# Performance work log

Hardware: AMD Instinct MI355X
Metric: run time of the kernel (lower is better)

The kernel has to match this reference:

```python
import jax, jax.numpy as jnp
import numpy as np

EPS = 1e-8

def setup_inputs() -> dict:
    key = jax.random.key(0)
    ks = jax.random.split(key, 10)
    N, IN, Z, C, H = 8192, 512, 128, 64, 50
    x = jax.random.normal(ks[0], (N, IN), dtype=jnp.float32)
    c = jax.random.randint(ks[1], (N, 1), 0, C, dtype=jnp.int64)
    z = jax.random.normal(ks[2], (N, Z), dtype=jnp.float32)
    # f_x MLP params (Linear(IN,50) -> ReLU -> Linear(50,Z))
    W1 = jax.random.normal(ks[3], (IN, H), dtype=jnp.float32) / np.sqrt(IN)
    b1 = jax.random.normal(ks[4], (H,), dtype=jnp.float32) * 0.01
    W2 = jax.random.normal(ks[5], (H, Z), dtype=jnp.float32) / np.sqrt(H)
    b2 = jax.random.normal(ks[6], (Z,), dtype=jnp.float32) * 0.01
    # f_z Linear(Z,Z)
    Wz = jax.random.normal(ks[7], (Z, Z), dtype=jnp.float32) / np.sqrt(Z)
    bz = jax.random.normal(ks[8], (Z,), dtype=jnp.float32) * 0.01
    # per-category bilinear weights w_s [C,Z,Z] (torch.randn init)
    Ws = jax.random.normal(ks[9], (C, Z, Z), dtype=jnp.float32)
    return {"x": x, "c": c, "z": z, "W1": W1, "b1": b1, "W2": W2, "b2": b2, "Wz": Wz, "bz": bz, "Ws": Ws}

def reference(x, c, z, W1, b1, W2, b2, Wz, bz, Ws):
    cf = c.reshape(-1)                                    # [N]
    fx = jax.nn.relu(x @ W1 + b1) @ W2 + b2               # [N,Z]
    fz = z @ Wz + bz                                      # [N,Z]
    # per-sample bilinear: u[n] = fx[n] @ Ws[c[n]]
    u = jnp.einsum('nd,nde->ne', fx, Ws[cf])              # [N,Z]
    T = jax.nn.softplus(jnp.einsum('ne,ne->n', u, fz))    # [N]
    # neg_T[i] = mean over j with c[j]==c[i] of softplus(fx[i] @ Ws[c[i]] @ fz[j])
    S = jax.nn.softplus(u @ fz.T)                         # [N,N]
    mask = (cf[:, None] == cf[None, :]).astype(S.dtype)   # [N,N]
    neg_T = (S * mask).sum(axis=1) / mask.sum(axis=1)     # [N]
    return jnp.log(T + EPS) - jnp.log(neg_T + EPS)
```

## Files before the change

### kernel.cpp

```cpp
#include <hip/hip_runtime.h>
#include <math.h>

#define N_   8192
#define IN_  512
#define ZD   128
#define CC   64
#define HD   50
#define EPSF 1e-8f

typedef float vf4 __attribute__((ext_vector_type(4)));
typedef __attribute__((ext_vector_type(8))) short bfrag;

#define MFMA16(a, b, c) __builtin_amdgcn_mfma_f32_16x16x32_bf16((a), (b), (c), 0, 0, 0)

__device__ __forceinline__ float softplus_hot(float t) {
    return fmaxf(t, 0.f) + __logf(1.f + __expf(-fabsf(t)));
}
__device__ __forceinline__ float softplus_acc(float t) {
    return fmaxf(t, 0.f) + log1pf(expf(-fabsf(t)));
}
__device__ __forceinline__ unsigned short bf16_rn(float x) {
    unsigned int u = __float_as_uint(x);
    return (unsigned short)((u + 0x7fff + ((u >> 16) & 1)) >> 16);
}
__device__ __forceinline__ float bf16_f(unsigned short h) {
    return __uint_as_float(((unsigned int)h) << 16);
}
__device__ __forceinline__ void split8(const float* v, bfrag& hi, bfrag& lo) {
    #pragma unroll
    for (int e = 0; e < 8; ++e) {
        unsigned short h = bf16_rn(v[e]);
        ((short*)&hi)[e] = (short)h;
        ((short*)&lo)[e] = (short)bf16_rn(v[e] - bf16_f(h));
    }
}

__global__ __launch_bounds__(256) void k_pre(const int* __restrict__ c,
                                             const float* __restrict__ W1,
                                             const float* __restrict__ z,
                                             const float* __restrict__ Wz,
                                             const float* __restrict__ bz,
                                             const float* __restrict__ W2,
                                             const float* __restrict__ Ws,
                                             uint4* __restrict__ W1p,
                                             uint4* __restrict__ W2p,
                                             float* __restrict__ fz,
                                             unsigned short* __restrict__ fz_hi,
                                             unsigned short* __restrict__ Wst_hi,
                                             unsigned short* __restrict__ Wst_lo,
                                             int* __restrict__ counts,
                                             int* __restrict__ offsets,
                                             int* __restrict__ grouped) {
    __shared__ float smem[64 * 129];
    int tid = threadIdx.x;
    int b   = blockIdx.x;
    if (b < CC) {
        __shared__ int hist[CC];
        __shared__ int cursor;
        __shared__ int off_s;
        if (tid < CC) hist[tid] = 0;
        if (tid == 0) cursor = 0;
        __syncthreads();
        for (int i = tid; i < N_; i += 256) atomicAdd(&hist[c[i]], 1);
        __syncthreads();
        if (tid == 0) {
            int off = 0;
            for (int q = 0; q < b; ++q) off += hist[q];
            off_s = off;
            counts[b]  = hist[b];
            offsets[b] = off;
        }
        __syncthreads();
        int off = off_s;
        for (int i = tid; i < N_; i += 256) {
            if (c[i] == b) {
                int p = atomicAdd(&cursor, 1);
                grouped[off + p] = i;
            }
        }
    } else if (b < 80) {
        int unit = (b - 64) * 256 + tid;
        int lane = unit & 63, f = (unit >> 6) & 15, kc = unit >> 10;
        int nt = f >> 2, ks = f & 3;
        int n = nt * 16 + (lane & 15);
        int kbase = kc * 128 + ks * 32 + (lane >> 4) * 8;
        unsigned short hi8[8], lo8[8];
        #pragma unroll
        for (int j = 0; j < 8; ++j) {
            int k = kbase + j;
            float v = (n < HD) ? W1[k * HD + n] : 0.f;
            unsigned short h = bf16_rn(v);
            hi8[j] = h;
            lo8[j] = bf16_rn(v - bf16_f(h));
        }
        W1p[kc * 2048 + f * 64 + lane]        = *(uint4*)hi8;
        W1p[kc * 2048 + 1024 + f * 64 + lane] = *(uint4*)lo8;
    } else if (b < 84) {
        int unit = (b - 80) * 256 + tid;
        int lane = unit & 63, f = unit >> 6;
        int nt = f >> 1, ks = f & 1;
        int n = nt * 16 + (lane & 15);
        int kbase = ks * 32 + (lane >> 4) * 8;
        unsigned short hi8[8], lo8[8];
        #pragma unroll
        for (int j = 0; j < 8; ++j) {
            int k = kbase + j;
            float v = (k < HD) ? W2[k * ZD + n] : 0.f;
            unsigned short h = bf16_rn(v);
            hi8[j] = h;
            lo8[j] = bf16_rn(v - bf16_f(h));
        }
        W2p[f * 64 + lane]        = *(uint4*)hi8;
        W2p[1024 + f * 64 + lane] = *(uint4*)lo8;
    } else if (b < 212) {
        float* sz = smem;
        int row0 = (b - 84) * 64;
        vf4* s4 = (vf4*)sz;
        const vf4* z4 = (const vf4*)(z + (size_t)row0 * ZD);
        #pragma unroll
        for (int f = 0; f < 8; ++f) s4[tid + f * 256] = z4[tid + f * 256];
        __syncthreads();
        int cp = tid & 31, rgp = tid >> 5;
        const vf4* Wz4 = (const vf4*)Wz;
        vf4 bb = ((const vf4*)bz)[cp];
        vf4 acc[8];
        #pragma unroll
        for (int r = 0; r < 8; ++r) acc[r] = bb;
        #pragma unroll 1
        for (int d4 = 0; d4 < 32; ++d4) {
            vf4 w0 = Wz4[(4 * d4 + 0) * 32 + cp];
            vf4 w1 = Wz4[(4 * d4 + 1) * 32 + cp];
            vf4 w2 = Wz4[(4 * d4 + 2) * 32 + cp];
            vf4 w3 = Wz4[(4 * d4 + 3) * 32 + cp];
            #pragma unroll
            for (int r = 0; r < 8; ++r) {
                vf4 a = s4[(rgp * 8 + r) * 32 + d4];
                acc[r] += a[0] * w0;
                acc[r] += a[1] * w1;
                acc[r] += a[2] * w2;
                acc[r] += a[3] * w3;
            }
        }
        vf4* fz4 = (vf4*)fz;
        #pragma unroll
        for (int r = 0; r < 8; ++r) {
            int n = row0 + rgp * 8 + r;
            fz4[(size_t)n * 32 + cp] = acc[r];
            ushort4 h;
            h.x = bf16_rn(acc[r][0]); h.y = bf16_rn(acc[r][1]);
            h.z = bf16_rn(acc[r][2]); h.w = bf16_rn(acc[r][3]);
            *(ushort4*)(fz_hi + (size_t)n * ZD + cp * 4) = h;
        }
    } else {
        #pragma unroll 1
        for (int ci = 0; ci < 2; ++ci) {
            int cat = (b - 212) * 2 + ci;
            const float* Wc = Ws + (size_t)cat * ZD * ZD;
            unsigned short* Whi = Wst_hi + (size_t)cat * ZD * ZD;
            unsigned short* Wlo = Wst_lo + (size_t)cat * ZD * ZD;
            #pragma unroll 1
            for (int half = 0; half < 2; ++half) {
                __syncthreads();
                const vf4* src = (const vf4*)(Wc + (size_t)half * 64 * ZD);
                #pragma unroll
                for (int f = 0; f < 8; ++f) {
                    int idx = tid + f * 256;
                    int row = idx >> 5, q = idx & 31;
                    vf4 v = src[idx];
                    #pragma unroll
                    for (int e = 0; e < 4; ++e) smem[row * 129 + q * 4 + e] = v[e];
                }
                __syncthreads();
                #pragma unroll 1
                for (int f = 0; f < 32; ++f) {
                    int idx = tid + f * 256;
                    int e = idx >> 6, dd = idx & 63;
                    float v = smem[dd * 129 + e];
                    unsigned short h = bf16_rn(v);
                    Whi[(size_t)e * ZD + half * 64 + dd] = h;
                    Wlo[(size_t)e * ZD + half * 64 + dd] = bf16_rn(v - bf16_f(h));
                }
            }
        }
    }
}

#define TI 8
__global__ __launch_bounds__(512) void k_all(const float* __restrict__ x,
                                             const uint4* __restrict__ W1p,
                                             const uint4* __restrict__ W2p,
                                             const float* __restrict__ b1,
                                             const float* __restrict__ b2,
                                             const unsigned short* __restrict__ Wst_hi,
                                             const unsigned short* __restrict__ Wst_lo,
                                             const float* __restrict__ fz,
                                             const unsigned short* __restrict__ fz_hi,
                                             const int* __restrict__ grouped,
                                             const int* __restrict__ offsets,
                                             const int* __restrict__ counts,
                                             float* __restrict__ out) {
    __shared__ __align__(16) unsigned char SM[78848];
    uint4* A4    = (uint4*)(SM);
    uint4* B4    = (uint4*)(SM + 34816);
    float* shC   = (float*)(SM + 69632);
    float* sRedF = (float*)(SM + 78336);

    int tid = threadIdx.x;
    int cat = blockIdx.x >> 3;
    int t   = blockIdx.x & (TI - 1);
    int off = offsets[cat], cnt = counts[cat];
    int i0 = t * 32;
    if (i0 >= cnt) return;
    int mI = min(32, cnt - i0);

    int lane = tid & 63, wave = tid >> 6;
    int m = lane & 15, quad = lane >> 4;
    int rg = wave & 1, ch = wave >> 1;

    uint4* sW2 = A4;
    uint4* sW1 = B4;
    float* sh  = shC;

    #pragma unroll
    for (int f = 0; f < 4; ++f) sW2[tid + f * 512] = W2p[tid + f * 512];

    int irowA = rg * 16 + m;
    int n_gA = grouped[off + i0 + min(irowA, mI - 1)];
    const float4* xr = (const float4*)(x + (size_t)n_gA * IN_);

    vf4 accP = {0.f, 0.f, 0.f, 0.f};
    vf4 accQ = {0.f, 0.f, 0.f, 0.f};
    vf4 accR = {0.f, 0.f, 0.f, 0.f};

    #pragma unroll 1
    for (int kc = 0; kc < 4; ++kc) {
        __syncthreads();
        #pragma unroll
        for (int f = 0; f < 4; ++f)
            sW1[tid + f * 512] = W1p[kc * 2048 + tid + f * 512];
        __syncthreads();
        #pragma unroll 1
        for (int ks = 0; ks < 4; ++ks) {
            float4 xa = xr[kc * 32 + ks * 8 + quad * 2];
            float4 xb = xr[kc * 32 + ks * 8 + quad * 2 + 1];
            float xv[8] = {xa.x, xa.y, xa.z, xa.w, xb.x, xb.y, xb.z, xb.w};
            bfrag ah, al;
            split8(xv, ah, al);
            bfrag bh = *(const bfrag*)&sW1[(ch * 4 + ks) * 64 + lane];
            bfrag bl = *(const bfrag*)&sW1[1024 + (ch * 4 + ks) * 64 + lane];
            accP = MFMA16(ah, bh, accP);
            accQ = MFMA16(ah, bl, accQ);
            accR = MFMA16(al, bh, accR);
        }
    }
    {
        int col = ch * 16 + m;
        float bb = (col < HD) ? b1[col] : 0.f;
        vf4 acc = accP + accQ + accR;
        #pragma unroll
        for (int r = 0; r < 4; ++r)
            sh[(rg * 16 + quad * 4 + r) * 68 + col] = fmaxf(acc[r] + bb, 0.f);
    }
    __syncthreads();

    bfrag ah2[2], al2[2];
    #pragma unroll
    for (int ks = 0; ks < 2; ++ks) {
        const float4* shp = (const float4*)&sh[(rg * 16 + m) * 68 + ks * 32 + quad * 8];
        float4 ha = shp[0], hb = shp[1];
        float hv[8] = {ha.x, ha.y, ha.z, ha.w, hb.x, hb.y, hb.z, hb.w};
        split8(hv, ah2[ks], al2[ks]);
    }
    __syncthreads();

    unsigned short* fxhiT = (unsigned short*)shC;
    unsigned short* fxloT = (unsigned short*)B4;
    #pragma unroll
    for (int nt2 = 0; nt2 < 2; ++nt2) {
        int nt = ch * 2 + nt2;
        bfrag bh0 = *(const bfrag*)&sW2[(nt * 2 + 0) * 64 + lane];
        bfrag bl0 = *(const bfrag*)&sW2[1024 + (nt * 2 + 0) * 64 + lane];
        bfrag bh1 = *(const bfrag*)&sW2[(nt * 2 + 1) * 64 + lane];
        bfrag bl1 = *(const bfrag*)&sW2[1024 + (nt * 2 + 1) * 64 + lane];
        vf4 aA = {0.f, 0.f, 0.f, 0.f}, aB = {0.f, 0.f, 0.f, 0.f};
        aA = MFMA16(ah2[0], bh0, aA);
        aA = MFMA16(ah2[0], bl0, aA);
        aA = MFMA16(al2[0], bh0, aA);
        aB = MFMA16(ah2[1], bh1, aB);
        aB = MFMA16(ah2[1], bl1, aB);
        aB = MFMA16(al2[1], bh1, aB);
        vf4 a2 = aA + aB;
        int colB = nt * 16 + m;
        float bb2 = b2[colB];
        #pragma unroll
        for (int r = 0; r < 4; ++r) {
            int row = rg * 16 + quad * 4 + r;
            float v = a2[r] + bb2;
            unsigned short hh = bf16_rn(v);
            fxhiT[row * 136 + colB] = hh;
            fxloT[row * 136 + colB] = bf16_rn(v - bf16_f(hh));
        }
    }
    __syncthreads();

    int eh = ch;
    bfrag a_hi[4], a_lo[4];
    #pragma unroll
    for (int kb = 0; kb < 4; ++kb) {
        a_hi[kb] = *(const bfrag*)&fxhiT[(rg * 16 + m) * 136 + kb * 32 + quad * 8];
        a_lo[kb] = *(const bfrag*)&fxloT[(rg * 16 + m) * 136 + kb * 32 + quad * 8];
    }
    __syncthreads();

    uint4* sWhi = A4;
    uint4* sWlo = B4;
    const uint4* gh = (const uint4*)(Wst_hi + (size_t)cat * ZD * ZD);
    const uint4* gl = (const uint4*)(Wst_lo + (size_t)cat * ZD * ZD);
    #pragma unroll
    for (int f = 0; f < 4; ++f) {
        int idx = tid + f * 512;
        int e = idx >> 4, q = idx & 15;
        sWhi[e * 17 + q] = gh[idx];
        sWlo[e * 17 + q] = gl[idx];
    }
    __syncthreads();

    vf4 uacc[2];
    #pragma unroll 1
    for (int et2 = 0; et2 < 2; ++et2) {
        int et = eh * 2 + et2;
        vf4 aH = {0.f, 0.f, 0.f, 0.f};
        vf4 aM = {0.f, 0.f, 0.f, 0.f};
        vf4 aL = {0.f, 0.f, 0.f, 0.f};
        #pragma unroll
        for (int kb = 0; kb < 4; ++kb) {
            bfrag bh = *(const bfrag*)&sWhi[(et * 16 + m) * 17 + kb * 4 + quad];
            bfrag bl = *(const bfrag*)&sWlo[(et * 16 + m) * 17 + kb * 4 + quad];
            aH = MFMA16(a_hi[kb], bh, aH);
            aM = MFMA16(a_hi[kb], bl, aM);
            aL = MFMA16(a_lo[kb], bh, aL);
        }
        uacc[et2] = aH + aM + aL;
    }

    int nrow[4];
    #pragma unroll
    for (int r = 0; r < 4; ++r) {
        int ir = rg * 16 + quad * 4 + r;
        nrow[r] = (ir < mI) ? grouped[off + i0 + ir] : -1;
    }
    float fzv[2][4];
    #pragma unroll
    for (int et2 = 0; et2 < 2; ++et2) {
        #pragma unroll
        for (int r = 0; r < 4; ++r) {
            fzv[et2][r] = 0.f;
            if (nrow[r] >= 0)
                fzv[et2][r] = fz[(size_t)nrow[r] * ZD + (eh * 2 + et2) * 16 + m];
        }
    }
    float p[4] = {0.f, 0.f, 0.f, 0.f};
    #pragma unroll
    for (int et2 = 0; et2 < 2; ++et2) {
        #pragma unroll
        for (int r = 0; r < 4; ++r) p[r] += uacc[et2][r] * fzv[et2][r];
    }
    #pragma unroll
    for (int r = 0; r < 4; ++r) {
        float v = p[r];
        #pragma unroll
        for (int s = 8; s >= 1; s >>= 1) v += __shfl_xor(v, s, 64);
        p[r] = v;
    }
    if (m == 0) {
        #pragma unroll
        for (int r = 0; r < 4; ++r)
            sRedF[(rg * 4 + eh) * 16 + quad * 4 + r] = p[r];
    }
    __syncthreads();

    unsigned short* su = (unsigned short*)A4;
    #pragma unroll
    for (int et2 = 0; et2 < 2; ++et2) {
        int col = (eh * 2 + et2) * 16 + m;
        #pragma unroll
        for (int r = 0; r < 4; ++r)
            su[(rg * 16 + quad * 4 + r) * 136 + col] = bf16_rn(uacc[et2][r]);
    }
    float logT_r[4] = {0.f, 0.f, 0.f, 0.f};
    if (eh == 0) {
        #pragma unroll
        for (int r = 0; r < 4; ++r) {
            float pt = sRedF[(rg * 4 + 0) * 16 + quad * 4 + r]
                     + sRedF[(rg * 4 + 1) * 16 + quad * 4 + r]
                     + sRedF[(rg * 4 + 2) * 16 + quad * 4 + r]
                     + sRedF[(rg * 4 + 3) * 16 + quad * 4 + r];
            logT_r[r] = logf(softplus_acc(pt) + EPSF);
        }
    }
    __syncthreads();

    bfrag na[4];
    #pragma unroll
    for (int kb = 0; kb < 4; ++kb)
        na[kb] = *(const bfrag*)&su[(rg * 16 + m) * 136 + kb * 32 + quad * 8];

    uint4* sB = B4;
    float negsum[4] = {0.f, 0.f, 0.f, 0.f};

    #pragma unroll 1
    for (int jb = 0; jb < cnt; jb += 64) {
        int mJ = min(64, cnt - jb);
        __syncthreads();
        #pragma unroll
        for (int f = 0; f < 2; ++f) {
            int idx = tid + f * 512;
            int jr = idx >> 4, q = idx & 15;
            uint4 v = {0u, 0u, 0u, 0u};
            if (jr < mJ) {
                int j_g = grouped[off + jb + jr];
                v = *(const uint4*)(fz_hi + (size_t)j_g * ZD + q * 8);
            }
            sB[jr * 17 + q] = v;
        }
        __syncthreads();
        {
            int jt = eh;
            bfrag b0 = *(const bfrag*)&sB[(jt * 16 + m) * 17 + 0 + quad];
            bfrag b1 = *(const bfrag*)&sB[(jt * 16 + m) * 17 + 4 + quad];
            bfrag b2 = *(const bfrag*)&sB[(jt * 16 + m) * 17 + 8 + quad];
            bfrag b3 = *(const bfrag*)&sB[(jt * 16 + m) * 17 + 12 + quad];
            vf4 aA = {0.f, 0.f, 0.f, 0.f}, aB = {0.f, 0.f, 0.f, 0.f};
            aA = MFMA16(na[0], b0, aA);
            aA = MFMA16(na[1], b1, aA);
            aB = MFMA16(na[2], b2, aB);
            aB = MFMA16(na[3], b3, aB);
            vf4 acc = aA + aB;
            bool jok = (jt * 16 + m) < mJ;
            #pragma unroll
            for (int r = 0; r < 4; ++r)
                if (jok) negsum[r] += softplus_hot(acc[r]);
        }
    }

    #pragma unroll
    for (int r = 0; r < 4; ++r) {
        float v = negsum[r];
        #pragma unroll
        for (int s = 8; s >= 1; s >>= 1) v += __shfl_xor(v, s, 64);
        negsum[r] = v;
    }
    if (m == 0) {
        #pragma unroll
        for (int r = 0; r < 4; ++r)
            sRedF[(rg * 4 + eh) * 16 + quad * 4 + r] = negsum[r];
    }
    __syncthreads();
    if (eh == 0 && m == 0) {
        #pragma unroll
        for (int r = 0; r < 4; ++r) {
            if (nrow[r] >= 0) {
                float tot = sRedF[(rg * 4 + 0) * 16 + quad * 4 + r]
                          + sRedF[(rg * 4 + 1) * 16 + quad * 4 + r]
                          + sRedF[(rg * 4 + 2) * 16 + quad * 4 + r]
                          + sRedF[(rg * 4 + 3) * 16 + quad * 4 + r];
                out[nrow[r]] = logT_r[r] - logf(tot / (float)cnt + EPSF);
            }
        }
    }
}

extern "C" void kernel_launch(void* const* d_in, const int* in_sizes, int n_in,
                              void* d_out, int out_size, void* d_ws, size_t ws_size,
                              hipStream_t stream) {
    const float* x  = (const float*)d_in[0];
    const int*   c  = (const int*)  d_in[1];
    const float* z  = (const float*)d_in[2];
    const float* W1 = (const float*)d_in[3];
    const float* b1 = (const float*)d_in[4];
    const float* W2 = (const float*)d_in[5];
    const float* b2 = (const float*)d_in[6];
    const float* Wz = (const float*)d_in[7];
    const float* bz = (const float*)d_in[8];
    const float* Ws = (const float*)d_in[9];
    float* out = (float*)d_out;

    uint4* W1p = (uint4*)d_ws;
    uint4* W2p = W1p + 8192;
    float* fz  = (float*)(W2p + 2048);
    unsigned short* fz_hi  = (unsigned short*)(fz + (size_t)N_ * ZD);
    unsigned short* Wst_hi = fz_hi + (size_t)N_ * ZD;
    unsigned short* Wst_lo = Wst_hi + (size_t)CC * ZD * ZD;
    int* counts  = (int*)(Wst_lo + (size_t)CC * ZD * ZD);
    int* offsets = counts + CC;
    int* grouped = offsets + CC;

    k_pre <<<244, 256, 0, stream>>>(c, W1, z, Wz, bz, W2, Ws, W1p, W2p, fz,
                                    fz_hi, Wst_hi, Wst_lo, counts, offsets,
                                    grouped);
    k_all <<<CC * TI, 512, 0, stream>>>(x, W1p, W2p, b1, b2, Wst_hi, Wst_lo,
                                        fz, fz_hi, grouped, offsets, counts,
                                        out);
}
```

Before: 132.2 us.

## Prefetch fz tiles and W1 chunks into registers, split Ws conversion across more blocks

```diff
diff --git a/kernel.cpp b/kernel.cpp
--- a/kernel.cpp
+++ b/kernel.cpp
@@ -29,7 +29,8 @@
 __device__ __forceinline__ void split8(const float* v, bfrag& hi, bfrag& lo) {
     #pragma unroll
     for (int e = 0; e < 8; ++e) {
-        unsigned short h = bf16_rn(v[e]);
+        unsigned int u = __float_as_uint(v[e]);
+        unsigned short h = (unsigned short)(u >> 16);
         ((short*)&hi)[e] = (short)h;
         ((short*)&lo)[e] = (short)bf16_rn(v[e] - bf16_f(h));
     }
@@ -152,34 +153,31 @@
             *(ushort4*)(fz_hi + (size_t)n * ZD + cp * 4) = h;
         }
     } else {
+        int cat = b - 212;
+        const float* Wc = Ws + (size_t)cat * ZD * ZD;
+        unsigned short* Whi = Wst_hi + (size_t)cat * ZD * ZD;
+        unsigned short* Wlo = Wst_lo + (size_t)cat * ZD * ZD;
         #pragma unroll 1
-        for (int ci = 0; ci < 2; ++ci) {
-            int cat = (b - 212) * 2 + ci;
-            const float* Wc = Ws + (size_t)cat * ZD * ZD;
-            unsigned short* Whi = Wst_hi + (size_t)cat * ZD * ZD;
-            unsigned short* Wlo = Wst_lo + (size_t)cat * ZD * ZD;
+        for (int half = 0; half < 2; ++half) {
+            __syncthreads();
+            const vf4* src = (const vf4*)(Wc + (size_t)half * 64 * ZD);
+            #pragma unroll
+            for (int f = 0; f < 8; ++f) {
+                int idx = tid + f * 256;
+                int row = idx >> 5, q = idx & 31;
+                vf4 v = src[idx];
+                #pragma unroll
+                for (int e = 0; e < 4; ++e) smem[row * 129 + q * 4 + e] = v[e];
+            }
+            __syncthreads();
             #pragma unroll 1
-            for (int half = 0; half < 2; ++half) {
-                __syncthreads();
-                const vf4* src = (const vf4*)(Wc + (size_t)half * 64 * ZD);
-                #pragma unroll
-                for (int f = 0; f < 8; ++f) {
-                    int idx = tid + f * 256;
-                    int row = idx >> 5, q = idx & 31;
-                    vf4 v = src[idx];
-                    #pragma unroll
-                    for (int e = 0; e < 4; ++e) smem[row * 129 + q * 4 + e] = v[e];
-                }
-                __syncthreads();
-                #pragma unroll 1
-                for (int f = 0; f < 32; ++f) {
-                    int idx = tid + f * 256;
-                    int e = idx >> 6, dd = idx & 63;
-                    float v = smem[dd * 129 + e];
-                    unsigned short h = bf16_rn(v);
-                    Whi[(size_t)e * ZD + half * 64 + dd] = h;
-                    Wlo[(size_t)e * ZD + half * 64 + dd] = bf16_rn(v - bf16_f(h));
-                }
+            for (int f = 0; f < 32; ++f) {
+                int idx = tid + f * 256;
+                int e = idx >> 6, dd = idx & 63;
+                float v = smem[dd * 129 + e];
+                unsigned short h = bf16_rn(v);
+                Whi[(size_t)e * ZD + half * 64 + dd] = h;
+                Wlo[(size_t)e * ZD + half * 64 + dd] = bf16_rn(v - bf16_f(h));
             }
         }
     }
@@ -234,12 +232,17 @@
 
     #pragma unroll 1
     for (int kc = 0; kc < 4; ++kc) {
-        __syncthreads();
-        #pragma unroll
-        for (int f = 0; f < 4; ++f)
-            sW1[tid + f * 512] = W1p[kc * 2048 + tid + f * 512];
-        __syncthreads();
-        #pragma unroll 1
+        uint4 w1r0 = W1p[kc * 2048 + tid];
+        uint4 w1r1 = W1p[kc * 2048 + tid + 512];
+        uint4 w1r2 = W1p[kc * 2048 + tid + 1024];
+        uint4 w1r3 = W1p[kc * 2048 + tid + 1536];
+        __syncthreads();
+        sW1[tid]        = w1r0;
+        sW1[tid + 512]  = w1r1;
+        sW1[tid + 1024] = w1r2;
+        sW1[tid + 1536] = w1r3;
+        __syncthreads();
+        #pragma unroll
         for (int ks = 0; ks < 4; ++ks) {
             float4 xa = xr[kc * 32 + ks * 8 + quad * 2];
             float4 xb = xr[kc * 32 + ks * 8 + quad * 2 + 1];
@@ -296,7 +299,8 @@
         for (int r = 0; r < 4; ++r) {
             int row = rg * 16 + quad * 4 + r;
             float v = a2[r] + bb2;
-            unsigned short hh = bf16_rn(v);
+            unsigned int u = __float_as_uint(v);
+            unsigned short hh = (unsigned short)(u >> 16);
             fxhiT[row * 136 + colB] = hh;
             fxloT[row * 136 + colB] = bf16_rn(v - bf16_f(hh));
         }
@@ -407,21 +411,42 @@
 
     uint4* sB = B4;
     float negsum[4] = {0.f, 0.f, 0.f, 0.f};
+    int jr_s = tid >> 4, q_s = tid & 15;
+
+    uint4 pf0, pf1;
+    {
+        int mJ0 = min(64, cnt);
+        uint4 v0 = {0u, 0u, 0u, 0u}, v1 = {0u, 0u, 0u, 0u};
+        if (jr_s < mJ0) {
+            int j_g = grouped[off + jr_s];
+            v0 = *(const uint4*)(fz_hi + (size_t)j_g * ZD + q_s * 8);
+        }
+        if (jr_s + 32 < mJ0) {
+            int j_g = grouped[off + jr_s + 32];
+            v1 = *(const uint4*)(fz_hi + (size_t)j_g * ZD + q_s * 8);
+        }
+        pf0 = v0; pf1 = v1;
+    }
 
     #pragma unroll 1
     for (int jb = 0; jb < cnt; jb += 64) {
         int mJ = min(64, cnt - jb);
         __syncthreads();
-        #pragma unroll
-        for (int f = 0; f < 2; ++f) {
-            int idx = tid + f * 512;
-            int jr = idx >> 4, q = idx & 15;
-            uint4 v = {0u, 0u, 0u, 0u};
-            if (jr < mJ) {
-                int j_g = grouped[off + jb + jr];
-                v = *(const uint4*)(fz_hi + (size_t)j_g * ZD + q * 8);
-            }
-            sB[jr * 17 + q] = v;
+        sB[jr_s * 17 + q_s]        = pf0;
+        sB[(jr_s + 32) * 17 + q_s] = pf1;
+        int jn = jb + 64;
+        if (jn < cnt) {
+            int mJn = min(64, cnt - jn);
+            uint4 v0 = {0u, 0u, 0u, 0u}, v1 = {0u, 0u, 0u, 0u};
+            if (jr_s < mJn) {
+                int j_g = grouped[off + jn + jr_s];
+                v0 = *(const uint4*)(fz_hi + (size_t)j_g * ZD + q_s * 8);
+            }
+            if (jr_s + 32 < mJn) {
+                int j_g = grouped[off + jn + jr_s + 32];
+                v1 = *(const uint4*)(fz_hi + (size_t)j_g * ZD + q_s * 8);
+            }
+            pf0 = v0; pf1 = v1;
         }
         __syncthreads();
         {
@@ -495,7 +520,7 @@
     int* offsets = counts + CC;
     int* grouped = offsets + CC;
 
-    k_pre <<<244, 256, 0, stream>>>(c, W1, z, Wz, bz, W2, Ws, W1p, W2p, fz,
+    k_pre <<<276, 256, 0, stream>>>(c, W1, z, Wz, bz, W2, Ws, W1p, W2p, fz,
                                     fz_hi, Wst_hi, Wst_lo, counts, offsets,
                                     grouped);
     k_all <<<CC * TI, 512, 0, stream>>>(x, W1p, W2p, b1, b2, Wst_hi, Wst_lo,
```

New measurement: 131.1 us. About the same (-0.8%).
